# Kernel tuning notes

Measured on AMD Instinct MI355X. Metric: run time of the kernel, lower is better.

Reference implementation:

```python
import jax, jax.numpy as jnp
import numpy as np

B, L, D = 32, 256, 1024
H = 8
DQ = D // H            # 128, dim_q == dim_k
DS = 64                # dim_s
DM = 256               # dim_mlp_s
DF = 4096              # dim_feedforward
EPS = 1e-5


def _layernorm(x, g, b):
    mu = jnp.mean(x, axis=-1, keepdims=True)
    var = jnp.mean(jnp.square(x - mu), axis=-1, keepdims=True)
    return (x - mu) * jax.lax.rsqrt(var + EPS) * g + b


def setup_inputs() -> dict:
    key = jax.random.key(0)
    ks = jax.random.split(key, 20)
    s = 0.02
    inp = {
        'src': jax.random.normal(ks[0], (B, L, D), jnp.float32),
        'sf': jax.random.normal(ks[1], (B, DS), jnp.float32),
        'atten_mask': jax.random.randint(ks[2], (B, L, L), 0, 2, jnp.int32),
        # per-head projections, stacked over heads (in,out layout)
        'qw': jax.random.normal(ks[3], (H, D, DQ), jnp.float32) * s,
        'qb': jnp.zeros((H, DQ), jnp.float32),
        'kw': jax.random.normal(ks[4], (H, D, DQ), jnp.float32) * s,
        'kb': jnp.zeros((H, DQ), jnp.float32),
        'vw': jax.random.normal(ks[5], (H, D, DQ), jnp.float32) * s,
        'vb': jnp.zeros((H, DQ), jnp.float32),
        # per-head bias MLP: dim_s -> dim_mlp_s -> L*L
        'b1w': jax.random.normal(ks[6], (H, DS, DM), jnp.float32) * s,
        'b1b': jnp.zeros((H, DM), jnp.float32),
        'b2w': jax.random.normal(ks[7], (H, DM, L * L), jnp.float32) * s,
        'b2b': jnp.zeros((H, L * L), jnp.float32),
        # output projection
        'ow': jax.random.normal(ks[8], (H * DQ, D), jnp.float32) * s,
        'ob': jnp.zeros((D,), jnp.float32),
        # layernorms
        'ln1_g': jnp.ones((D,), jnp.float32), 'ln1_b': jnp.zeros((D,), jnp.float32),
        'ln2_g': jnp.ones((D,), jnp.float32), 'ln2_b': jnp.zeros((D,), jnp.float32),
        # feed-forward
        'w1': jax.random.normal(ks[9], (D, DF), jnp.float32) * s,
        'bf1': jnp.zeros((DF,), jnp.float32),
        'w2': jax.random.normal(ks[10], (DF, D), jnp.float32) * s,
        'bf2': jnp.zeros((D,), jnp.float32),
    }
    return inp


def reference(src, sf, atten_mask, qw, qb, kw, kb, vw, vb, b1w, b1b, b2w, b2b,
              ow, ob, ln1_g, ln1_b, ln2_g, ln2_b, w1, bf1, w2, bf2):
    mask = atten_mask.astype(bool)                      # (B,L,L)
    # per-head projections: (H,B,L,DQ)
    q = jnp.einsum('bld,hdq->hblq', src, qw) + qb[:, None, None, :]
    k = jnp.einsum('bld,hdq->hblq', src, kw) + kb[:, None, None, :]
    v = jnp.einsum('bld,hdq->hblq', src, vw) + vb[:, None, None, :]
    scale = q.shape[-1] ** 0.5
    scores = jnp.einsum('hblq,hbmq->hblm', q, k) / scale
    # masked_fill with constant 1e-9 (NOT -inf), as in the original
    scores = jnp.where(mask[None], jnp.float32(1e-9), scores)
    # per-head learned bias from side features, added AFTER softmax
    hid = jax.nn.relu(jnp.einsum('bs,hsm->hbm', sf, b1w) + b1b[:, None, :])
    bias = (jnp.einsum('hbm,hmn->hbn', hid, b2w) + b2b[:, None, :]).reshape(H, B, L, L)
    soft = jax.nn.softmax(scores, axis=-1) + bias
    out = jnp.einsum('hblm,hbmv->hblv', soft, v)        # (H,B,L,DQ)
    # faithful to original: each head's result is indexed [0] -> batch element 0
    head0 = out[:, 0]                                   # (H,L,DQ)
    hidden = jnp.transpose(head0, (1, 0, 2)).reshape(L, H * DQ)
    attn = hidden @ ow + ob                             # (L,D), broadcasts over batch
    x = _layernorm(src + attn[None], ln1_g, ln1_b)      # (B,L,D)
    ffn = jax.nn.relu(x @ w1 + bf1) @ w2 + bf2
    return _layernorm(x + ffn, ln2_g, ln2_b)
```

## Files before the change

kernel.cpp:

```cpp
#include <hip/hip_runtime.h>

typedef unsigned short u16;
typedef short s16x8 __attribute__((ext_vector_type(8)));
typedef u16 u16x4 __attribute__((ext_vector_type(4)));
typedef float f32x4 __attribute__((ext_vector_type(4)));

#define B_ 32
#define L_ 256
#define D_ 1024
#define H_ 8
#define DQ_ 128
#define DS_ 64
#define DM_ 256
#define DF_ 4096

__device__ __forceinline__ u16 f2bf(float f) {
  unsigned u = __float_as_uint(f);
  unsigned r = (u + 0x7FFFu + ((u >> 16) & 1u)) >> 16;
  return (u16)r;
}
__device__ __forceinline__ float bf2f(u16 x) {
  return __uint_as_float(((unsigned)x) << 16);
}

__device__ __forceinline__ f32x4 mfma16(s16x8 a, s16x8 b, f32x4 c) {
  return __builtin_amdgcn_mfma_f32_16x16x32_bf16(a, b, c, 0, 0, 0);
}

#define GLDS16(g, l)                                                        \
  __builtin_amdgcn_global_load_lds(                                         \
      (__attribute__((address_space(1))) const void*)(g),                   \
      (__attribute__((address_space(3))) void*)(l), 16, 0, 0)

__device__ __forceinline__ void tile_tr(const float* __restrict__ ip,
                                        u16* __restrict__ op, int K, int N,
                                        int bx, int by, float (*t)[33], int tid) {
  const int tx = tid & 31, ty = tid >> 5;
  const long n0 = (long)bx * 32, k0 = (long)by * 32;
#pragma unroll
  for (int i = 0; i < 4; ++i)
    t[ty + i * 8][tx] = ip[(k0 + ty + i * 8) * (long)N + n0 + tx];
  __syncthreads();
#pragma unroll
  for (int i = 0; i < 4; ++i)
    op[(n0 + ty + i * 8) * (long)K + k0 + tx] = f2bf(t[tx][ty + i * 8]);
}

__global__ __launch_bounds__(256) void prep(
    const float* __restrict__ qw, const float* __restrict__ kw,
    const float* __restrict__ vw, const float* __restrict__ ow,
    const float* __restrict__ w1, const float* __restrict__ w2,
    const float* __restrict__ src, const float* __restrict__ sf,
    const float* __restrict__ b1w, const float* __restrict__ b1b,
    u16* __restrict__ qwT, u16* __restrict__ kwT, u16* __restrict__ vwT,
    u16* __restrict__ owT, u16* __restrict__ w1T, u16* __restrict__ w2T,
    u16* __restrict__ src0b, float* __restrict__ nzv, int* __restrict__ nzi,
    int* __restrict__ nzcnt) {
  const int b = blockIdx.x;
  const int tid = threadIdx.x;
  __shared__ float t[32][33];
  __shared__ float s_sf[DS_];
  __shared__ int wcnt[4];
  if (b < 3072) {
    const int z = b >> 7, rem = b & 127;
    const int sel = z >> 3, h = z & 7;
    const float* ip = (sel == 0 ? qw : (sel == 1 ? kw : vw)) + (long)h * D_ * DQ_;
    u16* op = (sel == 0 ? qwT : (sel == 1 ? kwT : vwT)) + (long)h * DQ_ * D_;
    tile_tr(ip, op, D_, DQ_, rem & 3, rem >> 2, t, tid);
  } else if (b < 4096) {
    const int rem = b - 3072;
    tile_tr(ow, owT, D_, D_, rem & 31, rem >> 5, t, tid);
  } else if (b < 8192) {
    const int rem = b - 4096;
    tile_tr(w1, w1T, D_, DF_, rem & 127, rem >> 7, t, tid);
  } else if (b < 12288) {
    const int rem = b - 8192;
    tile_tr(w2, w2T, DF_, D_, rem & 31, rem >> 5, t, tid);
  } else if (b < 12544) {
    const int rem = b - 12288;
    const int i = (rem * 256 + tid) * 4;
    float4 v = *(const float4*)(src + i);
    u16x4 o = {f2bf(v.x), f2bf(v.y), f2bf(v.z), f2bf(v.w)};
    *(u16x4*)(src0b + i) = o;
  } else {
    const int h = b - 12544;
    if (tid < DS_) s_sf[tid] = sf[tid];
    __syncthreads();
    float a = b1b[h * DM_ + tid];
    const float* wp = b1w + (long)h * DS_ * DM_ + tid;
#pragma unroll 8
    for (int s = 0; s < DS_; ++s) a += s_sf[s] * wp[s * DM_];
    a = fmaxf(a, 0.f);
    const unsigned long long bal = __ballot(a > 0.f);
    const int lane = tid & 63, wv = tid >> 6;
    const int pc = __popcll(bal);
    if (lane == 0) wcnt[wv] = pc;
    __syncthreads();
    int base = 0;
    for (int i = 0; i < wv; ++i) base += wcnt[i];
    const int pos = base + __popcll(bal & ((1ull << lane) - 1ull));
    if (a > 0.f) { nzv[h * DM_ + pos] = a; nzi[h * DM_ + pos] = tid; }
    if (tid == 255) nzcnt[h] = base + pc;
  }
}

__global__ __launch_bounds__(256) void phase2(
    const float* __restrict__ nzv, const int* __restrict__ nzi,
    const int* __restrict__ nzcnt, const float* __restrict__ b2w,
    const float* __restrict__ b2b, float* __restrict__ biasb,
    const u16* __restrict__ src0b, const u16* __restrict__ qwT,
    const u16* __restrict__ kwT, const u16* __restrict__ vwT,
    const float* __restrict__ qb, const float* __restrict__ kb,
    const float* __restrict__ vb, u16* __restrict__ q0, u16* __restrict__ k0,
    u16* __restrict__ v0T) {
  const int b = blockIdx.x;
  const int tid = threadIdx.x;
  __shared__ float sv[DM_];
  __shared__ int si[DM_];
  __shared__ u16 smA[128 * 32];
  __shared__ u16 smB[128 * 32];
  if (b < 512) {
    const int h = b >> 6;
    const int n0 = (b & 63) << 10;
    const int nnz = nzcnt[h];
    if (tid < DM_) { sv[tid] = nzv[h * DM_ + tid]; si[tid] = nzi[h * DM_ + tid]; }
    __syncthreads();
    const float* wb = b2w + (long)h * DM_ * 65536 + n0 + tid * 4;
    float4 acc = {0.f, 0.f, 0.f, 0.f};
    int j = 0;
    for (; j + 4 <= nnz; j += 4) {
      const float4 a0 = *(const float4*)(wb + (long)si[j] * 65536);
      const float4 a1 = *(const float4*)(wb + (long)si[j + 1] * 65536);
      const float4 a2 = *(const float4*)(wb + (long)si[j + 2] * 65536);
      const float4 a3 = *(const float4*)(wb + (long)si[j + 3] * 65536);
      const float v0 = sv[j], v1 = sv[j + 1], v2 = sv[j + 2], v3 = sv[j + 3];
      acc.x += v0 * a0.x + v1 * a1.x + v2 * a2.x + v3 * a3.x;
      acc.y += v0 * a0.y + v1 * a1.y + v2 * a2.y + v3 * a3.y;
      acc.z += v0 * a0.z + v1 * a1.z + v2 * a2.z + v3 * a3.z;
      acc.w += v0 * a0.w + v1 * a1.w + v2 * a2.w + v3 * a3.w;
    }
    for (; j < nnz; ++j) {
      const float4 a0 = *(const float4*)(wb + (long)si[j] * 65536);
      const float v0 = sv[j];
      acc.x += v0 * a0.x; acc.y += v0 * a0.y; acc.z += v0 * a0.z; acc.w += v0 * a0.w;
    }
    const float4 bb = *(const float4*)(b2b + (long)h * 65536 + n0 + tid * 4);
    float4 o = {acc.x + bb.x, acc.y + bb.y, acc.z + bb.z, acc.w + bb.w};
    *(float4*)(biasb + (long)h * 65536 + n0 + tid * 4) = o;
  } else {
    const int r = b - 512;
    const int z = r >> 1, sel = z >> 3, h = z & 7;
    const long tm = (long)(r & 1) * 128;
    const int K = D_;
    const u16* BT = (sel == 0 ? qwT : (sel == 1 ? kwT : vwT)) + (long)h * DQ_ * D_;
    const float* bias = (sel == 0 ? qb : (sel == 1 ? kb : vb)) + h * DQ_;
    const int lane = tid & 63;
    const int wv = tid >> 6;
    const int wr = wv >> 1, wc = wv & 1;
    const u16* ga = src0b + (tm + (tid >> 2)) * (long)K + (tid & 3) * 8;
    const u16* gb = BT + (long)(tid >> 2) * K + (tid & 3) * 8;
    const long rstep = 64L * K;
    u16* la = &smA[tid * 8];
    u16* lb = &smB[tid * 8];
    f32x4 acc[4][4];
#pragma unroll
    for (int m = 0; m < 4; ++m)
#pragma unroll
      for (int n = 0; n < 4; ++n) acc[m][n] = (f32x4){0.f, 0.f, 0.f, 0.f};
    for (int k0_ = 0; k0_ < K; k0_ += 32) {
      GLDS16(ga + k0_, la);
      GLDS16(ga + rstep + k0_, la + 64 * 32);
      GLDS16(gb + k0_, lb);
      GLDS16(gb + rstep + k0_, lb + 64 * 32);
      __syncthreads();
      s16x8 af[4], bf[4];
      const int ka = (lane >> 4) * 8;
      const int ra = wr * 64 + (lane & 15);
      const int rb = wc * 64 + (lane & 15);
#pragma unroll
      for (int m = 0; m < 4; ++m) af[m] = *(const s16x8*)&smA[(ra + m * 16) * 32 + ka];
#pragma unroll
      for (int n = 0; n < 4; ++n) bf[n] = *(const s16x8*)&smB[(rb + n * 16) * 32 + ka];
#pragma unroll
      for (int m = 0; m < 4; ++m)
#pragma unroll
        for (int n = 0; n < 4; ++n) acc[m][n] = mfma16(af[m], bf[n], acc[m][n]);
      __syncthreads();
    }
    const long crow0 = tm + wr * 64 + ((lane >> 4) * 4);
    const long ccol0 = wc * 64 + (lane & 15);
#pragma unroll
    for (int m = 0; m < 4; ++m) {
#pragma unroll
      for (int n = 0; n < 4; ++n) {
#pragma unroll
        for (int i = 0; i < 4; ++i) {
          const long row = crow0 + m * 16 + i;
          const long col = ccol0 + n * 16;
          const float v = acc[m][n][i] + bias[col];
          if (sel < 2) {
            u16* o = (sel == 0 ? q0 : k0) + (long)h * L_ * DQ_;
            o[row * DQ_ + col] = f2bf(v);
          } else {
            v0T[(long)h * DQ_ * L_ + col * L_ + row] = f2bf(v);
          }
        }
      }
    }
  }
}

__global__ __launch_bounds__(256) void gemm_bt(
    const u16* __restrict__ A, const u16* __restrict__ BT, float* __restrict__ C,
    const float* __restrict__ bias, int K, int ldc) {
  __shared__ u16 smA[128 * 32];
  __shared__ u16 smB[128 * 32];
  const int tid = threadIdx.x;
  const int lane = tid & 63;
  const int wv = tid >> 6;
  const int wr = wv >> 1, wc = wv & 1;
  const long tm = (long)blockIdx.x * 128;
  const long tn = (long)blockIdx.y * 128;

  const u16* ga = A + (tm + (tid >> 2)) * (long)K + (tid & 3) * 8;
  const u16* gb = BT + (tn + (tid >> 2)) * (long)K + (tid & 3) * 8;
  const long rstep = 64L * K;
  u16* la = &smA[tid * 8];
  u16* lb = &smB[tid * 8];

  f32x4 acc[4][4];
#pragma unroll
  for (int m = 0; m < 4; ++m)
#pragma unroll
    for (int n = 0; n < 4; ++n) acc[m][n] = (f32x4){0.f, 0.f, 0.f, 0.f};

  for (int k0 = 0; k0 < K; k0 += 32) {
    GLDS16(ga + k0, la);
    GLDS16(ga + rstep + k0, la + 64 * 32);
    GLDS16(gb + k0, lb);
    GLDS16(gb + rstep + k0, lb + 64 * 32);
    __syncthreads();
    s16x8 af[4], bf[4];
    const int ka = (lane >> 4) * 8;
    const int ra = wr * 64 + (lane & 15);
    const int rb = wc * 64 + (lane & 15);
#pragma unroll
    for (int m = 0; m < 4; ++m) af[m] = *(const s16x8*)&smA[(ra + m * 16) * 32 + ka];
#pragma unroll
    for (int n = 0; n < 4; ++n) bf[n] = *(const s16x8*)&smB[(rb + n * 16) * 32 + ka];
#pragma unroll
    for (int m = 0; m < 4; ++m)
#pragma unroll
      for (int n = 0; n < 4; ++n) acc[m][n] = mfma16(af[m], bf[n], acc[m][n]);
    __syncthreads();
  }

  const long crow0 = tm + wr * 64 + ((lane >> 4) * 4);
  const long ccol0 = tn + wc * 64 + (lane & 15);
#pragma unroll
  for (int m = 0; m < 4; ++m)
#pragma unroll
    for (int n = 0; n < 4; ++n)
#pragma unroll
      for (int i = 0; i < 4; ++i) {
        const long row = crow0 + m * 16 + i;
        const long col = ccol0 + n * 16;
        C[row * (long)ldc + col] = acc[m][n][i] + bias[col];
      }
}

template <int BN, int EPI>
__global__ __launch_bounds__(512, 2) void gemm8p(
    const u16* __restrict__ A, const u16* __restrict__ BT, void* __restrict__ Cv,
    const float* __restrict__ bias, const void* __restrict__ R, int M, int N,
    int K, int ldc) {
  extern __shared__ char lds[];
  constexpr int NR = BN / 64;
  constexpr int NHB = BN / 128;
  constexpr int BUF = 32768 + BN * 128;
  constexpr int WST = (NHB == 2) ? 4 : 2;
  const int tid = threadIdx.x;
  const int lane = tid & 63;
  const int w = tid >> 6;
  const int wr = w >> 2, wc = w & 3;

  const int total = gridDim.x;
  int bid = blockIdx.x;
  int s = ((total & 7) == 0) ? ((bid & 7) * (total >> 3) + (bid >> 3)) : bid;
  const int gn = N / BN;
  const long tm = (long)(s / gn) * 256;
  const long tn = (long)(s % gn) * BN;
  const int NT = K >> 6;

  auto stageA = [&](int half, int t) {
    char* hb = lds + (long)(t & 1) * BUF + half * 16384;
    const u16* g = A + (tm + half * 128) * (long)K + (long)t * 64;
#pragma unroll
    for (int j = 0; j < 2; ++j) {
      const int idx = j * 512 + tid;
      const int r = idx >> 3;
      const int c16 = (idx & 7) ^ (r & 7);
      GLDS16(g + (long)r * K + c16 * 8, hb + idx * 16);
    }
  };
  auto stageB = [&](int half, int t) {
    char* hb = lds + (long)(t & 1) * BUF + 32768 + half * 16384;
    const u16* g = BT + (tn + half * 128) * (long)K + (long)t * 64;
#pragma unroll
    for (int j = 0; j < 2; ++j) {
      const int idx = j * 512 + tid;
      const int r = idx >> 3;
      const int c16 = (idx & 7) ^ (r & 7);
      GLDS16(g + (long)r * K + c16 * 8, hb + idx * 16);
    }
  };

  stageA(0, 0);
  stageA(1, 0);
  stageB(0, 0);
  if (NHB == 2) stageB(1, 0);
  stageB(0, 1);
  if (NHB == 2) stageB(1, 1);
  asm volatile("s_waitcnt vmcnt(%0)" ::"n"(WST) : "memory");
  __builtin_amdgcn_s_barrier();

  f32x4 acc[8][NR];
#pragma unroll
  for (int m = 0; m < 8; ++m)
#pragma unroll
    for (int n = 0; n < NR; ++n) acc[m][n] = (f32x4){0.f, 0.f, 0.f, 0.f};

  const int lk = (lane >> 4) * 16;
  const int lr = lane & 15;

  for (int t = 0; t < NT; ++t) {
    const char* bp = lds + (long)(t & 1) * BUF;
    s16x8 bfr[NR][2];
#pragma unroll
    for (int p = 0; p < 4; ++p) {
      if (p == 0) {
#pragma unroll
        for (int ni = 0; ni < NR; ++ni) {
          const int brow = wc * (BN / 4) + ni * 16 + lr;
#pragma unroll
          for (int ks = 0; ks < 2; ++ks) {
            const int kb = (ks * 64 + lk) ^ ((brow & 7) << 4);
            bfr[ni][ks] = *(const s16x8*)(bp + 32768 + brow * 128 + kb);
          }
        }
      }
      s16x8 afr[2][2];
#pragma unroll
      for (int rI = 0; rI < 2; ++rI) {
        const int arow = wr * 128 + (2 * p + rI) * 16 + lr;
#pragma unroll
        for (int ks = 0; ks < 2; ++ks) {
          const int kb = (ks * 64 + lk) ^ ((arow & 7) << 4);
          afr[rI][ks] = *(const s16x8*)(bp + arow * 128 + kb);
        }
      }
      if (p == 0) {
        if (t + 1 < NT) stageA(0, t + 1);
      } else if (p == 1) {
        if (t + 1 < NT) stageA(1, t + 1);
      } else if (p == 2) {
        if (t + 2 < NT) stageB(0, t + 2);
      } else {
        if (NHB == 2 && t + 2 < NT) stageB(1, t + 2);
      }
      __builtin_amdgcn_s_barrier();
      __builtin_amdgcn_s_setprio(1);
#pragma unroll
      for (int rI = 0; rI < 2; ++rI)
#pragma unroll
        for (int ni = 0; ni < NR; ++ni)
#pragma unroll
          for (int ks = 0; ks < 2; ++ks)
            acc[2 * p + rI][ni] = mfma16(afr[rI][ks], bfr[ni][ks], acc[2 * p + rI][ni]);
      __builtin_amdgcn_s_setprio(0);
      if (p == 3) {
        if (t + 2 < NT) {
          asm volatile("s_waitcnt vmcnt(%0)" ::"n"(WST) : "memory");
        } else if (t + 1 < NT) {
          asm volatile("s_waitcnt vmcnt(0)" ::: "memory");
        }
      }
      __builtin_amdgcn_s_barrier();
    }
  }

  const long crow0 = tm + wr * 128 + ((lane >> 4) * 4);
  const long ccol0 = tn + wc * (BN / 4) + lr;
#pragma unroll
  for (int m = 0; m < 8; ++m) {
#pragma unroll
    for (int n = 0; n < NR; ++n) {
#pragma unroll
      for (int i = 0; i < 4; ++i) {
        const long row = crow0 + m * 16 + i;
        const long col = ccol0 + n * 16;
        const float v = acc[m][n][i] + bias[col];
        if constexpr (EPI == 1) {
          ((u16*)Cv)[row * (long)ldc + col] = f2bf(fmaxf(v, 0.f));
        } else {
          const float r = bf2f(((const u16*)R)[row * (long)ldc + col]);
          ((u16*)Cv)[row * (long)ldc + col] = f2bf(v + r);
        }
      }
    }
  }
}

__global__ __launch_bounds__(64) void attn_kernel(
    const u16* __restrict__ q0, const u16* __restrict__ k0,
    const u16* __restrict__ vT, const float* __restrict__ biasb,
    const int* __restrict__ mask0, u16* __restrict__ hidden) {
  const int lane = threadIdx.x;
  const int h = blockIdx.y;
  const int r0 = blockIdx.x * 16;
  const u16* q = q0 + (long)h * L_ * DQ_;
  const u16* k = k0 + (long)h * L_ * DQ_;
  const u16* v = vT + (long)h * DQ_ * L_;
  const int lg = lane >> 4;
  const int ll = lane & 15;

  s16x8 aq[4];
#pragma unroll
  for (int kk = 0; kk < 4; ++kk)
    aq[kk] = *(const s16x8*)(q + (long)(r0 + ll) * DQ_ + kk * 32 + lg * 8);

  float sc[16][4];
  const float scale = 0.08838834764831845f;
#pragma unroll
  for (int t = 0; t < 16; ++t) {
    f32x4 a = {0.f, 0.f, 0.f, 0.f};
#pragma unroll
    for (int kk = 0; kk < 4; ++kk) {
      s16x8 bf = *(const s16x8*)(k + (long)(t * 16 + ll) * DQ_ + kk * 32 + lg * 8);
      a = mfma16(aq[kk], bf, a);
    }
#pragma unroll
    for (int i = 0; i < 4; ++i) {
      const int row = r0 + lg * 4 + i;
      const int col = t * 16 + ll;
      float s = a[i] * scale;
      if (mask0[row * L_ + col] != 0) s = 1e-9f;
      sc[t][i] = s;
    }
  }
#pragma unroll
  for (int i = 0; i < 4; ++i) {
    float mx = sc[0][i];
#pragma unroll
    for (int t = 1; t < 16; ++t) mx = fmaxf(mx, sc[t][i]);
#pragma unroll
    for (int d = 1; d < 16; d <<= 1) mx = fmaxf(mx, __shfl_xor(mx, d));
    float sum = 0.f;
#pragma unroll
    for (int t = 0; t < 16; ++t) {
      const float e = __expf(sc[t][i] - mx);
      sc[t][i] = e;
      sum += e;
    }
#pragma unroll
    for (int d = 1; d < 16; d <<= 1) sum += __shfl_xor(sum, d);
    const float inv = 1.f / sum;
    const int row = r0 + lg * 4 + i;
#pragma unroll
    for (int t = 0; t < 16; ++t)
      sc[t][i] = sc[t][i] * inv + biasb[(long)h * 65536 + (long)row * 256 + t * 16 + ll];
  }
  __shared__ float sm[16 * 256];
#pragma unroll
  for (int t = 0; t < 16; ++t)
#pragma unroll
    for (int i = 0; i < 4; ++i)
      sm[(lg * 4 + i) * 256 + t * 16 + ll] = sc[t][i];
  __syncthreads();
  s16x8 af[8];
#pragma unroll
  for (int kk = 0; kk < 8; ++kk) {
    const float* ap = &sm[ll * 256 + kk * 32 + lg * 8];
    s16x8 t8;
#pragma unroll
    for (int j = 0; j < 8; ++j) t8[j] = (short)f2bf(ap[j]);
    af[kk] = t8;
  }
#pragma unroll
  for (int n = 0; n < 8; ++n) {
    f32x4 a = {0.f, 0.f, 0.f, 0.f};
#pragma unroll
    for (int kk = 0; kk < 8; ++kk) {
      s16x8 bf = *(const s16x8*)(v + (long)(n * 16 + ll) * 256 + kk * 32 + lg * 8);
      a = mfma16(af[kk], bf, a);
    }
#pragma unroll
    for (int i = 0; i < 4; ++i) {
      const int row = r0 + lg * 4 + i;
      const int col = n * 16 + ll;
      hidden[(long)row * 1024 + h * 128 + col] = f2bf(a[i]);
    }
  }
}

template <int MODE>
__global__ __launch_bounds__(256) void ln_kernel(
    const void* __restrict__ in0v, const float* __restrict__ add1,
    const float* __restrict__ g, const float* __restrict__ bb,
    void* __restrict__ outv) {
  const int tid = threadIdx.x;
  const long row = blockIdx.x;
  float4 v;
  if constexpr (MODE == 0) {
    v = ((const float4*)((const float*)in0v + row * D_))[tid];
    const float4 u = ((const float4*)(add1 + (row & (L_ - 1)) * D_))[tid];
    v.x += u.x; v.y += u.y; v.z += u.z; v.w += u.w;
  } else {
    const uint2 pk = *(const uint2*)((const u16*)in0v + row * D_ + tid * 4);
    v.x = __uint_as_float((pk.x & 0xFFFFu) << 16);
    v.y = __uint_as_float(pk.x & 0xFFFF0000u);
    v.z = __uint_as_float((pk.y & 0xFFFFu) << 16);
    v.w = __uint_as_float(pk.y & 0xFFFF0000u);
  }
  float s = v.x + v.y + v.z + v.w;
  float q = v.x * v.x + v.y * v.y + v.z * v.z + v.w * v.w;
#pragma unroll
  for (int d = 1; d < 64; d <<= 1) { s += __shfl_xor(s, d); q += __shfl_xor(q, d); }
  __shared__ float ss[4], sq[4];
  const int wv = tid >> 6;
  if ((tid & 63) == 0) { ss[wv] = s; sq[wv] = q; }
  __syncthreads();
  s = ss[0] + ss[1] + ss[2] + ss[3];
  q = sq[0] + sq[1] + sq[2] + sq[3];
  const float mu = s * (1.f / D_);
  const float var = q * (1.f / D_) - mu * mu;
  const float rs = rsqrtf(var + 1e-5f);
  const float4 gv = ((const float4*)g)[tid];
  const float4 bv = ((const float4*)bb)[tid];
  float4 o;
  o.x = (v.x - mu) * rs * gv.x + bv.x;
  o.y = (v.y - mu) * rs * gv.y + bv.y;
  o.z = (v.z - mu) * rs * gv.z + bv.z;
  o.w = (v.w - mu) * rs * gv.w + bv.w;
  if constexpr (MODE == 0) {
    uint2 pk;
    pk.x = (unsigned)f2bf(o.x) | ((unsigned)f2bf(o.y) << 16);
    pk.y = (unsigned)f2bf(o.z) | ((unsigned)f2bf(o.w) << 16);
    *(uint2*)((u16*)outv + row * D_ + tid * 4) = pk;
  } else {
    ((float4*)((float*)outv + row * D_))[tid] = o;
  }
}

extern "C" void kernel_launch(void* const* d_in, const int* in_sizes, int n_in,
                              void* d_out, int out_size, void* d_ws, size_t ws_size,
                              hipStream_t stream) {
  (void)in_sizes; (void)n_in; (void)out_size; (void)ws_size;
  const float* src = (const float*)d_in[0];
  const float* sf = (const float*)d_in[1];
  const int* mask = (const int*)d_in[2];
  const float* qw = (const float*)d_in[3];
  const float* qb = (const float*)d_in[4];
  const float* kw = (const float*)d_in[5];
  const float* kb = (const float*)d_in[6];
  const float* vw = (const float*)d_in[7];
  const float* vb = (const float*)d_in[8];
  const float* b1w = (const float*)d_in[9];
  const float* b1b = (const float*)d_in[10];
  const float* b2w = (const float*)d_in[11];
  const float* b2b = (const float*)d_in[12];
  const float* ow = (const float*)d_in[13];
  const float* ob = (const float*)d_in[14];
  const float* ln1g = (const float*)d_in[15];
  const float* ln1b = (const float*)d_in[16];
  const float* ln2g = (const float*)d_in[17];
  const float* ln2b = (const float*)d_in[18];
  const float* w1 = (const float*)d_in[19];
  const float* bf1 = (const float*)d_in[20];
  const float* w2 = (const float*)d_in[21];
  const float* bf2 = (const float*)d_in[22];
  float* out = (float*)d_out;

  char* ws = (char*)d_ws;
  size_t off = 0;
  auto alloc = [&](size_t bytes) {
    void* p = ws + off;
    off += (bytes + 255) & ~(size_t)255;
    return p;
  };
  u16* qwT = (u16*)alloc((size_t)H_ * DQ_ * D_ * 2);
  u16* kwT = (u16*)alloc((size_t)H_ * DQ_ * D_ * 2);
  u16* vwT = (u16*)alloc((size_t)H_ * DQ_ * D_ * 2);
  u16* owT = (u16*)alloc((size_t)D_ * D_ * 2);
  u16* w1T = (u16*)alloc((size_t)DF_ * D_ * 2);
  u16* w2T = (u16*)alloc((size_t)D_ * DF_ * 2);
  u16* src0b = (u16*)alloc((size_t)L_ * D_ * 2);
  u16* q0 = (u16*)alloc((size_t)H_ * L_ * DQ_ * 2);
  u16* k0 = (u16*)alloc((size_t)H_ * L_ * DQ_ * 2);
  u16* v0T = (u16*)alloc((size_t)H_ * DQ_ * L_ * 2);
  float* nzv = (float*)alloc((size_t)H_ * DM_ * 4);
  int* nzi = (int*)alloc((size_t)H_ * DM_ * 4);
  int* nzcnt = (int*)alloc(256);
  float* biasb = (float*)alloc((size_t)H_ * L_ * L_ * 4);
  u16* hidden = (u16*)alloc((size_t)L_ * H_ * DQ_ * 2);
  float* attnvec = (float*)alloc((size_t)L_ * D_ * 4);
  u16* xb = (u16*)alloc((size_t)B_ * L_ * D_ * 2);
  u16* ffnh = (u16*)alloc((size_t)B_ * L_ * DF_ * 2);
  u16* yb = (u16*)alloc((size_t)B_ * L_ * D_ * 2);

  hipFuncSetAttribute((const void*)gemm8p<256, 1>,
                      hipFuncAttributeMaxDynamicSharedMemorySize, 131072);
  hipFuncSetAttribute((const void*)gemm8p<128, 2>,
                      hipFuncAttributeMaxDynamicSharedMemorySize, 98304);

  const dim3 b256(256);
  prep<<<dim3(12552), b256, 0, stream>>>(qw, kw, vw, ow, w1, w2, src, sf, b1w, b1b,
                                         qwT, kwT, vwT, owT, w1T, w2T, src0b, nzv,
                                         nzi, nzcnt);
  phase2<<<dim3(560), b256, 0, stream>>>(nzv, nzi, nzcnt, b2w, b2b, biasb, src0b,
                                         qwT, kwT, vwT, qb, kb, vb, q0, k0, v0T);
  attn_kernel<<<dim3(16, H_), dim3(64), 0, stream>>>(q0, k0, v0T, biasb, mask, hidden);
  gemm_bt<<<dim3(2, 8), b256, 0, stream>>>(hidden, owT, attnvec, ob, D_, D_);
  ln_kernel<0><<<dim3(B_ * L_), b256, 0, stream>>>(src, attnvec, ln1g, ln1b, xb);
  gemm8p<256, 1><<<dim3(512), dim3(512), 131072, stream>>>(
      xb, w1T, ffnh, bf1, nullptr, B_ * L_, DF_, D_, DF_);
  gemm8p<128, 2><<<dim3(256), dim3(512), 98304, stream>>>(
      ffnh, w2T, yb, bf2, xb, B_ * L_, D_, DF_, D_);
  ln_kernel<1><<<dim3(B_ * L_), b256, 0, stream>>>(yb, nullptr, ln2g, ln2b, out);
}
```

Before: 329.0 us.

## Fuse attention with output projection and move weight transposes into phase2

```diff
diff --git a/kernel.cpp b/kernel.cpp
--- a/kernel.cpp
+++ b/kernel.cpp
@@ -48,14 +48,11 @@
 
 __global__ __launch_bounds__(256) void prep(
     const float* __restrict__ qw, const float* __restrict__ kw,
-    const float* __restrict__ vw, const float* __restrict__ ow,
-    const float* __restrict__ w1, const float* __restrict__ w2,
-    const float* __restrict__ src, const float* __restrict__ sf,
-    const float* __restrict__ b1w, const float* __restrict__ b1b,
-    u16* __restrict__ qwT, u16* __restrict__ kwT, u16* __restrict__ vwT,
-    u16* __restrict__ owT, u16* __restrict__ w1T, u16* __restrict__ w2T,
-    u16* __restrict__ src0b, float* __restrict__ nzv, int* __restrict__ nzi,
-    int* __restrict__ nzcnt) {
+    const float* __restrict__ vw, const float* __restrict__ src,
+    const float* __restrict__ sf, const float* __restrict__ b1w,
+    const float* __restrict__ b1b, u16* __restrict__ qwT, u16* __restrict__ kwT,
+    u16* __restrict__ vwT, u16* __restrict__ src0b, float* __restrict__ nzv,
+    int* __restrict__ nzi, int* __restrict__ nzcnt) {
   const int b = blockIdx.x;
   const int tid = threadIdx.x;
   __shared__ float t[32][33];
@@ -67,23 +64,14 @@
     const float* ip = (sel == 0 ? qw : (sel == 1 ? kw : vw)) + (long)h * D_ * DQ_;
     u16* op = (sel == 0 ? qwT : (sel == 1 ? kwT : vwT)) + (long)h * DQ_ * D_;
     tile_tr(ip, op, D_, DQ_, rem & 3, rem >> 2, t, tid);
-  } else if (b < 4096) {
+  } else if (b < 3328) {
     const int rem = b - 3072;
-    tile_tr(ow, owT, D_, D_, rem & 31, rem >> 5, t, tid);
-  } else if (b < 8192) {
-    const int rem = b - 4096;
-    tile_tr(w1, w1T, D_, DF_, rem & 127, rem >> 7, t, tid);
-  } else if (b < 12288) {
-    const int rem = b - 8192;
-    tile_tr(w2, w2T, DF_, D_, rem & 31, rem >> 5, t, tid);
-  } else if (b < 12544) {
-    const int rem = b - 12288;
     const int i = (rem * 256 + tid) * 4;
     float4 v = *(const float4*)(src + i);
     u16x4 o = {f2bf(v.x), f2bf(v.y), f2bf(v.z), f2bf(v.w)};
     *(u16x4*)(src0b + i) = o;
   } else {
-    const int h = b - 12544;
+    const int h = b - 3328;
     if (tid < DS_) s_sf[tid] = sf[tid];
     __syncthreads();
     float a = b1b[h * DM_ + tid];
@@ -112,13 +100,16 @@
     const u16* __restrict__ kwT, const u16* __restrict__ vwT,
     const float* __restrict__ qb, const float* __restrict__ kb,
     const float* __restrict__ vb, u16* __restrict__ q0, u16* __restrict__ k0,
-    u16* __restrict__ v0T) {
+    u16* __restrict__ v0T, const float* __restrict__ ow,
+    const float* __restrict__ w1, const float* __restrict__ w2,
+    u16* __restrict__ owT, u16* __restrict__ w1T, u16* __restrict__ w2T) {
   const int b = blockIdx.x;
   const int tid = threadIdx.x;
   __shared__ float sv[DM_];
   __shared__ int si[DM_];
   __shared__ u16 smA[128 * 32];
   __shared__ u16 smB[128 * 32];
+  __shared__ float t[32][33];
   if (b < 512) {
     const int h = b >> 6;
     const int n0 = (b & 63) << 10;
@@ -147,7 +138,7 @@
     const float4 bb = *(const float4*)(b2b + (long)h * 65536 + n0 + tid * 4);
     float4 o = {acc.x + bb.x, acc.y + bb.y, acc.z + bb.z, acc.w + bb.w};
     *(float4*)(biasb + (long)h * 65536 + n0 + tid * 4) = o;
-  } else {
+  } else if (b < 560) {
     const int r = b - 512;
     const int z = r >> 1, sel = z >> 3, h = z & 7;
     const long tm = (long)(r & 1) * 128;
@@ -190,9 +181,9 @@
     const long crow0 = tm + wr * 64 + ((lane >> 4) * 4);
     const long ccol0 = wc * 64 + (lane & 15);
 #pragma unroll
-    for (int m = 0; m < 4; ++m) {
-#pragma unroll
-      for (int n = 0; n < 4; ++n) {
+    for (int m = 0; m < 4; ++m)
+#pragma unroll
+      for (int n = 0; n < 4; ++n)
 #pragma unroll
         for (int i = 0; i < 4; ++i) {
           const long row = crow0 + m * 16 + i;
@@ -205,68 +196,132 @@
             v0T[(long)h * DQ_ * L_ + col * L_ + row] = f2bf(v);
           }
         }
-      }
-    }
-  }
-}
-
-__global__ __launch_bounds__(256) void gemm_bt(
-    const u16* __restrict__ A, const u16* __restrict__ BT, float* __restrict__ C,
-    const float* __restrict__ bias, int K, int ldc) {
-  __shared__ u16 smA[128 * 32];
-  __shared__ u16 smB[128 * 32];
+  } else if (b < 1584) {
+    const int rem = b - 560;
+    tile_tr(ow, owT, D_, D_, rem & 31, rem >> 5, t, tid);
+  } else if (b < 5680) {
+    const int rem = b - 1584;
+    tile_tr(w1, w1T, D_, DF_, rem & 127, rem >> 7, t, tid);
+  } else {
+    const int rem = b - 5680;
+    tile_tr(w2, w2T, DF_, D_, rem & 31, rem >> 5, t, tid);
+  }
+}
+
+__global__ __launch_bounds__(512) void attnproj(
+    const u16* __restrict__ q0, const u16* __restrict__ k0,
+    const u16* __restrict__ v0T, const float* __restrict__ biasb,
+    const int* __restrict__ mask, const u16* __restrict__ owT,
+    const float* __restrict__ ob, float* __restrict__ attnvec) {
+  extern __shared__ char alds[];
   const int tid = threadIdx.x;
+  const int h = tid >> 6;
   const int lane = tid & 63;
-  const int wv = tid >> 6;
-  const int wr = wv >> 1, wc = wv & 1;
-  const long tm = (long)blockIdx.x * 128;
-  const long tn = (long)blockIdx.y * 128;
-
-  const u16* ga = A + (tm + (tid >> 2)) * (long)K + (tid & 3) * 8;
-  const u16* gb = BT + (tn + (tid >> 2)) * (long)K + (tid & 3) * 8;
-  const long rstep = 64L * K;
-  u16* la = &smA[tid * 8];
-  u16* lb = &smB[tid * 8];
-
-  f32x4 acc[4][4];
-#pragma unroll
-  for (int m = 0; m < 4; ++m)
-#pragma unroll
-    for (int n = 0; n < 4; ++n) acc[m][n] = (f32x4){0.f, 0.f, 0.f, 0.f};
-
-  for (int k0 = 0; k0 < K; k0 += 32) {
-    GLDS16(ga + k0, la);
-    GLDS16(ga + rstep + k0, la + 64 * 32);
-    GLDS16(gb + k0, lb);
-    GLDS16(gb + rstep + k0, lb + 64 * 32);
-    __syncthreads();
-    s16x8 af[4], bf[4];
-    const int ka = (lane >> 4) * 8;
-    const int ra = wr * 64 + (lane & 15);
-    const int rb = wc * 64 + (lane & 15);
-#pragma unroll
-    for (int m = 0; m < 4; ++m) af[m] = *(const s16x8*)&smA[(ra + m * 16) * 32 + ka];
-#pragma unroll
-    for (int n = 0; n < 4; ++n) bf[n] = *(const s16x8*)&smB[(rb + n * 16) * 32 + ka];
-#pragma unroll
-    for (int m = 0; m < 4; ++m)
-#pragma unroll
-      for (int n = 0; n < 4; ++n) acc[m][n] = mfma16(af[m], bf[n], acc[m][n]);
-    __syncthreads();
-  }
-
-  const long crow0 = tm + wr * 64 + ((lane >> 4) * 4);
-  const long ccol0 = tn + wc * 64 + (lane & 15);
-#pragma unroll
-  for (int m = 0; m < 4; ++m)
-#pragma unroll
-    for (int n = 0; n < 4; ++n)
-#pragma unroll
-      for (int i = 0; i < 4; ++i) {
-        const long row = crow0 + m * 16 + i;
-        const long col = ccol0 + n * 16;
-        C[row * (long)ldc + col] = acc[m][n][i] + bias[col];
-      }
+  const int lg = lane >> 4;
+  const int ll = lane & 15;
+  const int r0 = blockIdx.x * 16;
+
+  const u16* q = q0 + (long)h * L_ * DQ_;
+  const u16* k = k0 + (long)h * L_ * DQ_;
+  s16x8 aq[4];
+#pragma unroll
+  for (int kk = 0; kk < 4; ++kk)
+    aq[kk] = *(const s16x8*)(q + (long)(r0 + ll) * DQ_ + kk * 32 + lg * 8);
+  float sc[16][4];
+  const float scale = 0.08838834764831845f;
+#pragma unroll
+  for (int t = 0; t < 16; ++t) {
+    f32x4 a = {0.f, 0.f, 0.f, 0.f};
+#pragma unroll
+    for (int kk = 0; kk < 4; ++kk) {
+      s16x8 bf = *(const s16x8*)(k + (long)(t * 16 + ll) * DQ_ + kk * 32 + lg * 8);
+      a = mfma16(aq[kk], bf, a);
+    }
+#pragma unroll
+    for (int i = 0; i < 4; ++i) {
+      const int row = r0 + lg * 4 + i;
+      const int col = t * 16 + ll;
+      float s = a[i] * scale;
+      if (mask[row * L_ + col] != 0) s = 1e-9f;
+      sc[t][i] = s;
+    }
+  }
+#pragma unroll
+  for (int i = 0; i < 4; ++i) {
+    float mx = sc[0][i];
+#pragma unroll
+    for (int t = 1; t < 16; ++t) mx = fmaxf(mx, sc[t][i]);
+#pragma unroll
+    for (int d = 1; d < 16; d <<= 1) mx = fmaxf(mx, __shfl_xor(mx, d));
+    float sum = 0.f;
+#pragma unroll
+    for (int t = 0; t < 16; ++t) {
+      const float e = __expf(sc[t][i] - mx);
+      sc[t][i] = e;
+      sum += e;
+    }
+#pragma unroll
+    for (int d = 1; d < 16; d <<= 1) sum += __shfl_xor(sum, d);
+    const float inv = 1.f / sum;
+    const int row = r0 + lg * 4 + i;
+#pragma unroll
+    for (int t = 0; t < 16; ++t)
+      sc[t][i] = sc[t][i] * inv + biasb[(long)h * 65536 + (long)row * 256 + t * 16 + ll];
+  }
+  char* pbuf = alds + h * 8192;
+#pragma unroll
+  for (int t = 0; t < 16; ++t)
+#pragma unroll
+    for (int i = 0; i < 4; ++i) {
+      const int lr = lg * 4 + i;
+      const int cb = (t * 16 + ll) * 2;
+      *(u16*)(pbuf + lr * 512 + (cb ^ ((lr & 7) << 4))) = f2bf(sc[t][i]);
+    }
+  const u16* v = v0T + (long)h * DQ_ * L_;
+  char* hidb = alds + 65536;
+#pragma unroll
+  for (int kk = 0; kk < 8; ++kk) {
+  }
+  s16x8 paf[8];
+#pragma unroll
+  for (int kk = 0; kk < 8; ++kk)
+    paf[kk] = *(const s16x8*)(pbuf + ll * 512 + ((kk * 64 + lg * 16) ^ ((ll & 7) << 4)));
+#pragma unroll
+  for (int n = 0; n < 8; ++n) {
+    f32x4 a = {0.f, 0.f, 0.f, 0.f};
+#pragma unroll
+    for (int kk = 0; kk < 8; ++kk) {
+      s16x8 bf = *(const s16x8*)(v + (long)(n * 16 + ll) * 256 + kk * 32 + lg * 8);
+      a = mfma16(paf[kk], bf, a);
+    }
+#pragma unroll
+    for (int i = 0; i < 4; ++i) {
+      const int lr = lg * 4 + i;
+      const int cb = (h * 128 + n * 16 + ll) * 2;
+      *(u16*)(hidb + lr * 2048 + (cb ^ ((lr & 7) << 4))) = f2bf(a[i]);
+    }
+  }
+  __syncthreads();
+  f32x4 acc[8];
+#pragma unroll
+  for (int f = 0; f < 8; ++f) acc[f] = (f32x4){0.f, 0.f, 0.f, 0.f};
+#pragma unroll 2
+  for (int k0_ = 0; k0_ < 1024; k0_ += 32) {
+    const s16x8 af = *(const s16x8*)(hidb + ll * 2048 + ((k0_ * 2 + lg * 16) ^ ((ll & 7) << 4)));
+#pragma unroll
+    for (int f = 0; f < 8; ++f) {
+      const s16x8 bf = *(const s16x8*)(owT + (long)(h * 128 + f * 16 + ll) * 1024 + k0_ + lg * 8);
+      acc[f] = mfma16(af, bf, acc[f]);
+    }
+  }
+#pragma unroll
+  for (int f = 0; f < 8; ++f)
+#pragma unroll
+    for (int i = 0; i < 4; ++i) {
+      const int row = r0 + lg * 4 + i;
+      const int col = h * 128 + f * 16 + ll;
+      attnvec[(long)row * D_ + col] = acc[f][i] + ob[col];
+    }
 }
 
 template <int BN, int EPI>
@@ -359,15 +414,10 @@
           afr[rI][ks] = *(const s16x8*)(bp + arow * 128 + kb);
         }
       }
-      if (p == 0) {
-        if (t + 1 < NT) stageA(0, t + 1);
-      } else if (p == 1) {
-        if (t + 1 < NT) stageA(1, t + 1);
-      } else if (p == 2) {
-        if (t + 2 < NT) stageB(0, t + 2);
-      } else {
-        if (NHB == 2 && t + 2 < NT) stageB(1, t + 2);
-      }
+      if (p == 0) { if (t + 1 < NT) stageA(0, t + 1); }
+      else if (p == 1) { if (t + 1 < NT) stageA(1, t + 1); }
+      else if (p == 2) { if (t + 2 < NT) stageB(0, t + 2); }
+      else { if (NHB == 2 && t + 2 < NT) stageB(1, t + 2); }
       __builtin_amdgcn_s_barrier();
       __builtin_amdgcn_s_setprio(1);
 #pragma unroll
@@ -407,98 +457,6 @@
           ((u16*)Cv)[row * (long)ldc + col] = f2bf(v + r);
         }
       }
-    }
-  }
-}
-
-__global__ __launch_bounds__(64) void attn_kernel(
-    const u16* __restrict__ q0, const u16* __restrict__ k0,
-    const u16* __restrict__ vT, const float* __restrict__ biasb,
-    const int* __restrict__ mask0, u16* __restrict__ hidden) {
-  const int lane = threadIdx.x;
-  const int h = blockIdx.y;
-  const int r0 = blockIdx.x * 16;
-  const u16* q = q0 + (long)h * L_ * DQ_;
-  const u16* k = k0 + (long)h * L_ * DQ_;
-  const u16* v = vT + (long)h * DQ_ * L_;
-  const int lg = lane >> 4;
-  const int ll = lane & 15;
-
-  s16x8 aq[4];
-#pragma unroll
-  for (int kk = 0; kk < 4; ++kk)
-    aq[kk] = *(const s16x8*)(q + (long)(r0 + ll) * DQ_ + kk * 32 + lg * 8);
-
-  float sc[16][4];
-  const float scale = 0.08838834764831845f;
-#pragma unroll
-  for (int t = 0; t < 16; ++t) {
-    f32x4 a = {0.f, 0.f, 0.f, 0.f};
-#pragma unroll
-    for (int kk = 0; kk < 4; ++kk) {
-      s16x8 bf = *(const s16x8*)(k + (long)(t * 16 + ll) * DQ_ + kk * 32 + lg * 8);
-      a = mfma16(aq[kk], bf, a);
-    }
-#pragma unroll
-    for (int i = 0; i < 4; ++i) {
-      const int row = r0 + lg * 4 + i;
-      const int col = t * 16 + ll;
-      float s = a[i] * scale;
-      if (mask0[row * L_ + col] != 0) s = 1e-9f;
-      sc[t][i] = s;
-    }
-  }
-#pragma unroll
-  for (int i = 0; i < 4; ++i) {
-    float mx = sc[0][i];
-#pragma unroll
-    for (int t = 1; t < 16; ++t) mx = fmaxf(mx, sc[t][i]);
-#pragma unroll
-    for (int d = 1; d < 16; d <<= 1) mx = fmaxf(mx, __shfl_xor(mx, d));
-    float sum = 0.f;
-#pragma unroll
-    for (int t = 0; t < 16; ++t) {
-      const float e = __expf(sc[t][i] - mx);
-      sc[t][i] = e;
-      sum += e;
-    }
-#pragma unroll
-    for (int d = 1; d < 16; d <<= 1) sum += __shfl_xor(sum, d);
-    const float inv = 1.f / sum;
-    const int row = r0 + lg * 4 + i;
-#pragma unroll
-    for (int t = 0; t < 16; ++t)
-      sc[t][i] = sc[t][i] * inv + biasb[(long)h * 65536 + (long)row * 256 + t * 16 + ll];
-  }
-  __shared__ float sm[16 * 256];
-#pragma unroll
-  for (int t = 0; t < 16; ++t)
-#pragma unroll
-    for (int i = 0; i < 4; ++i)
-      sm[(lg * 4 + i) * 256 + t * 16 + ll] = sc[t][i];
-  __syncthreads();
-  s16x8 af[8];
-#pragma unroll
-  for (int kk = 0; kk < 8; ++kk) {
-    const float* ap = &sm[ll * 256 + kk * 32 + lg * 8];
-    s16x8 t8;
-#pragma unroll
-    for (int j = 0; j < 8; ++j) t8[j] = (short)f2bf(ap[j]);
-    af[kk] = t8;
-  }
-#pragma unroll
-  for (int n = 0; n < 8; ++n) {
-    f32x4 a = {0.f, 0.f, 0.f, 0.f};
-#pragma unroll
-    for (int kk = 0; kk < 8; ++kk) {
-      s16x8 bf = *(const s16x8*)(v + (long)(n * 16 + ll) * 256 + kk * 32 + lg * 8);
-      a = mfma16(af[kk], bf, a);
-    }
-#pragma unroll
-    for (int i = 0; i < 4; ++i) {
-      const int row = r0 + lg * 4 + i;
-      const int col = n * 16 + ll;
-      hidden[(long)row * 1024 + h * 128 + col] = f2bf(a[i]);
     }
   }
 }
@@ -602,7 +560,6 @@
   int* nzi = (int*)alloc((size_t)H_ * DM_ * 4);
   int* nzcnt = (int*)alloc(256);
   float* biasb = (float*)alloc((size_t)H_ * L_ * L_ * 4);
-  u16* hidden = (u16*)alloc((size_t)L_ * H_ * DQ_ * 2);
   float* attnvec = (float*)alloc((size_t)L_ * D_ * 4);
   u16* xb = (u16*)alloc((size_t)B_ * L_ * D_ * 2);
   u16* ffnh = (u16*)alloc((size_t)B_ * L_ * DF_ * 2);
@@ -612,15 +569,17 @@
                       hipFuncAttributeMaxDynamicSharedMemorySize, 131072);
   hipFuncSetAttribute((const void*)gemm8p<128, 2>,
                       hipFuncAttributeMaxDynamicSharedMemorySize, 98304);
+  hipFuncSetAttribute((const void*)attnproj,
+                      hipFuncAttributeMaxDynamicSharedMemorySize, 98304);
 
   const dim3 b256(256);
-  prep<<<dim3(12552), b256, 0, stream>>>(qw, kw, vw, ow, w1, w2, src, sf, b1w, b1b,
-                                         qwT, kwT, vwT, owT, w1T, w2T, src0b, nzv,
-                                         nzi, nzcnt);
-  phase2<<<dim3(560), b256, 0, stream>>>(nzv, nzi, nzcnt, b2w, b2b, biasb, src0b,
-                                         qwT, kwT, vwT, qb, kb, vb, q0, k0, v0T);
-  attn_kernel<<<dim3(16, H_), dim3(64), 0, stream>>>(q0, k0, v0T, biasb, mask, hidden);
-  gemm_bt<<<dim3(2, 8), b256, 0, stream>>>(hidden, owT, attnvec, ob, D_, D_);
+  prep<<<dim3(3336), b256, 0, stream>>>(qw, kw, vw, src, sf, b1w, b1b, qwT, kwT,
+                                        vwT, src0b, nzv, nzi, nzcnt);
+  phase2<<<dim3(9776), b256, 0, stream>>>(nzv, nzi, nzcnt, b2w, b2b, biasb, src0b,
+                                          qwT, kwT, vwT, qb, kb, vb, q0, k0, v0T,
+                                          ow, w1, w2, owT, w1T, w2T);
+  attnproj<<<dim3(16), dim3(512), 98304, stream>>>(q0, k0, v0T, biasb, mask, owT,
+                                                   ob, attnvec);
   ln_kernel<0><<<dim3(B_ * L_), b256, 0, stream>>>(src, attnvec, ln1g, ln1b, xb);
   gemm8p<256, 1><<<dim3(512), dim3(512), 131072, stream>>>(
       xb, w1T, ffnh, bf1, nullptr, B_ * L_, DF_, D_, DF_);
```

After: 356.5 us. 8.4% more time.
